# Kernel optimization log

Hardware: AMD Instinct MI355X
Metric: run time of the kernel (lower is better)

## Reference

```python
import jax, jax.numpy as jnp
import numpy as np

C, T, V, H, DQ = 64, 128, 25, 3, 32  # channels, frames, joints, heads, qkv_dim
EPS = 1e-5
LRELU_SLOPE = 0.1


def pos_embed(channels, num_frames, num_joints):
    # DSTA-Net style sinusoidal Pos_Embed: position index is the joint id, tiled over frames
    pos = np.tile(np.arange(num_joints, dtype=np.float32), num_frames)[:, None]  # (T*V, 1)
    div = np.exp(np.arange(0, channels, 2, dtype=np.float32) * -(np.log(10000.0) / channels))
    pe = np.zeros((num_frames * num_joints, channels), dtype=np.float32)
    pe[:, 0::2] = np.sin(pos * div)
    pe[:, 1::2] = np.cos(pos * div)
    pe = pe.reshape(num_frames, num_joints, channels).transpose(2, 0, 1)[None]  # (1, C, T, V)
    return jnp.asarray(pe)


def batchnorm2d(x, gamma, beta):
    # training-mode BN over (N, T, V) per channel, biased variance (torch default)
    m = x.mean(axis=(0, 2, 3), keepdims=True)
    v = x.var(axis=(0, 2, 3), keepdims=True)
    return (x - m) * jax.lax.rsqrt(v + EPS) * gamma[None, :, None, None] + beta[None, :, None, None]


def setup_inputs() -> dict:
    key = jax.random.key(0)
    ks = jax.random.split(key, 4)
    N = 64
    return {
        "x": jax.random.normal(ks[0], (N, C, T, V), jnp.float32),
        "Wqkv": jax.random.normal(ks[1], (2 * H * DQ, C), jnp.float32) * 0.05,   # 1x1 conv weight
        "bqkv": jnp.zeros((2 * H * DQ,), jnp.float32),
        "alphas": jnp.ones((1, H, 1, 1), jnp.float32),
        "att0s": jax.random.uniform(ks[2], (1, H, V, V), jnp.float32) / V,
        "Wout": jax.random.normal(ks[3], (C, H * C, 1, 5), jnp.float32) * 0.02,  # (1,5) temporal conv
        "bout": jnp.zeros((C,), jnp.float32),
        "gamma": jnp.ones((C,), jnp.float32),
        "beta": jnp.zeros((C,), jnp.float32),
    }


def reference(x, Wqkv, bqkv, alphas, att0s, Wout, bout, gamma, beta):
    N = x.shape[0]
    xs = x + pos_embed(C, T, V)                                   # pes(x) + x
    qk = jnp.einsum('nctv,oc->notv', xs, Wqkv) + bqkv[None, :, None, None]
    qk = qk.reshape(N, 2 * H, DQ, T, V)
    q, k = qk[:, :H], qk[:, H:]
    # tanh-gated joint-attention, no softmax
    att = jnp.tanh(jnp.einsum('nhctu,nhctv->nhuv', q, k) / (DQ * T)) * alphas + att0s
    y = jnp.einsum('nctu,nhuv->nhctv', x, att).reshape(N, H * C, T, V)
    y = jax.lax.conv_general_dilated(
        y, Wout, window_strides=(1, 1), padding=((0, 0), (2, 2)),
        dimension_numbers=('NCHW', 'OIHW', 'NCHW')) + bout[None, :, None, None]
    y = batchnorm2d(y, gamma, beta)
    return jax.nn.leaky_relu(y + x, LRELU_SLOPE)                  # ress is identity (in==out)
```

## Files before the change

kernel.cpp:

```cpp
#include <hip/hip_runtime.h>
#include <hip/hip_bf16.h>


#define WS_ATT    0
#define WS_STATS  120000
#define WS_WBF    120128
#define WS_WP     150848
#define WS_BP     156992
#define WS_PE     157184
#define WS_SPART  158784
#define WS_ATTBF  166976

typedef __attribute__((ext_vector_type(8))) short short8;
typedef __attribute__((ext_vector_type(4))) float floatx4;

__device__ __forceinline__ float us2f(unsigned short u) {
    union { unsigned int i; float f; } w; w.i = ((unsigned int)u) << 16; return w.f;
}
__device__ __forceinline__ unsigned short f2us(float f) {
    __hip_bfloat16_raw r = __float2bfloat16(f); return r.x;
}

__device__ __forceinline__ int swz(int col, int byteoff) {
    return col * 128 + ((((byteoff >> 4) ^ (col & 7)) << 4) | (byteoff & 15));
}

__device__ __forceinline__ void bar_lgkm() {
    asm volatile("s_waitcnt lgkmcnt(0)" ::: "memory");
    __builtin_amdgcn_s_barrier();
}

__global__ void k_wprep(const float* __restrict__ Wout, const float* __restrict__ Wqkv,
                        const float* __restrict__ bqkv, unsigned short* __restrict__ Abf,
                        unsigned short* __restrict__ Wp, float* __restrict__ bp,
                        float* __restrict__ pe)
{
    int i = blockIdx.x * 256 + threadIdx.x;
    if (i < 61440) {
        int tap = i / 12288, rem = i % 12288;
        int o = rem / 192, hc = rem % 192;
        Abf[i] = f2us(Wout[o * 960 + hc * 5 + tap]);
    } else if (i < 73728) {
        int j = i - 61440;
        int np = j >> 6, c = j & 63;
        int h = np >> 6, qk = (np >> 5) & 1, cp = np & 31;
        Wp[j] = f2us(Wqkv[(qk * 96 + h * 32 + cp) * 64 + c]);
    } else if (i < 73920) {
        int np = i - 73728;
        int h = np >> 6, qk = (np >> 5) & 1, cp = np & 31;
        bp[np] = bqkv[qk * 96 + h * 32 + cp];
    } else if (i < 75520) {
        int e = i - 73920;
        int c = e / 25, v = e % 25;
        int ii = c >> 1;
        float d = expf(-(float)(2 * ii) * (9.210340371976184f / 64.0f));
        float a = (float)v * d;
        pe[e] = (c & 1) ? cosf(a) : sinf(a);
    }
}

#define CPAD 112

__global__ __launch_bounds__(256, 2) void k_att(
    const float* __restrict__ x, const unsigned short* __restrict__ Wp,
    const float* __restrict__ bp, float* __restrict__ att_raw)
{
    __shared__ unsigned short xs_s[CPAD * 64];
    __shared__ unsigned short qk_s[3 * CPAD * 64];
    __shared__ float pe_s[1600];
    __shared__ float att_s[1875];

    const int tid  = threadIdx.x;
    const int lane = tid & 63, wv = tid >> 6;
    const int l16  = lane & 15, quad = lane >> 4;
    const int n    = blockIdx.y;
    const int tb0  = blockIdx.x * 16;

    for (int e = tid; e < 1600; e += 256) {
        int c = e / 25, v = e % 25;
        int i = c >> 1;
        float d = expf(-(float)(2 * i) * (9.210340371976184f / 64.0f));
        float a = (float)v * d;
        pe_s[e] = (c & 1) ? cosf(a) : sinf(a);
    }
    for (int e = tid; e < 1875; e += 256) att_s[e] = 0.0f;

    short8 afrag[3][2];
    float  biasr[3][4];
    #pragma unroll
    for (int mt = 0; mt < 3; ++mt) {
        int row = (3 * wv + mt) * 16 + l16;
        #pragma unroll
        for (int kk = 0; kk < 2; ++kk)
            afrag[mt][kk] = *(const short8*)(Wp + row * 64 + kk * 32 + quad * 8);
        #pragma unroll
        for (int reg = 0; reg < 4; ++reg)
            biasr[mt][reg] = bp[(3 * wv + mt) * 16 + quad * 4 + reg];
    }

    floatx4 qacc[3][2][2];
    #pragma unroll
    for (int h = 0; h < 3; ++h)
        #pragma unroll
        for (int a = 0; a < 2; ++a)
            #pragma unroll
            for (int b = 0; b < 2; ++b)
                qacc[h][a][b] = (floatx4){0.0f, 0.0f, 0.0f, 0.0f};

    const int col_a = lane;
    const int col_b = 64 + lane;
    const int va = (col_a < 25) ? col_a : (col_a < 50 ? col_a - 25 : col_a - 50);
    const int vb = (col_b < 75) ? col_b - 50 : col_b - 75;
    char* xsb = (char*)xs_s;
    char* qkb = (char*)qk_s;

    __syncthreads();

    for (int ch = 0; ch < 4; ++ch) {
        const int g0 = (tb0 + ch * 4) * 25;

        #pragma unroll
        for (int cp8 = 0; cp8 < 8; ++cp8) {
            const int cpair = wv * 8 + cp8;
            const int c0 = cpair * 2;
            const float* xp0 = x + (size_t)(n * 64 + c0) * 3200 + g0;
            const float* xp1 = xp0 + 3200;
            {
                unsigned int pk =
                    (unsigned int)f2us(xp0[col_a] + pe_s[c0 * 25 + va]) |
                    ((unsigned int)f2us(xp1[col_a] + pe_s[c0 * 25 + 25 + va]) << 16);
                *(unsigned int*)(xsb + swz(col_a, cpair * 4)) = pk;
            }
            if (lane < 36) {
                unsigned int pk =
                    (unsigned int)f2us(xp0[col_b] + pe_s[c0 * 25 + vb]) |
                    ((unsigned int)f2us(xp1[col_b] + pe_s[c0 * 25 + 25 + vb]) << 16);
                *(unsigned int*)(xsb + swz(col_b, cpair * 4)) = pk;
            }
        }
        __syncthreads();

        #pragma unroll
        for (int nt = 0; nt < 7; ++nt) {
            const int col = nt * 16 + l16;
            short8 b0 = *(const short8*)(xsb + swz(col, quad * 16));
            short8 b1 = *(const short8*)(xsb + swz(col, 64 + quad * 16));
            #pragma unroll
            for (int mt = 0; mt < 3; ++mt) {
                floatx4 acc = (floatx4){0.0f, 0.0f, 0.0f, 0.0f};
                acc = __builtin_amdgcn_mfma_f32_16x16x32_bf16(afrag[mt][0], b0, acc, 0, 0, 0);
                acc = __builtin_amdgcn_mfma_f32_16x16x32_bf16(afrag[mt][1], b1, acc, 0, 0, 0);
                const int np  = (3 * wv + mt) * 16 + quad * 4;
                const int h   = np >> 6;
                const int off = (np & 63) * 2;
                unsigned long long pk =
                      (unsigned long long)f2us(acc[0] + biasr[mt][0])
                    | ((unsigned long long)f2us(acc[1] + biasr[mt][1]) << 16)
                    | ((unsigned long long)f2us(acc[2] + biasr[mt][2]) << 32)
                    | ((unsigned long long)f2us(acc[3] + biasr[mt][3]) << 48);
                *(unsigned long long*)(qkb + h * (CPAD * 128) + swz(col, off)) = pk;
            }
        }
        __syncthreads();

        const int tcol = wv * 25;
        #pragma unroll
        for (int h = 0; h < 3; ++h) {
            char* qh = qkb + h * (CPAD * 128);
            short8 qa0 = *(const short8*)(qh + swz(tcol + l16,      quad * 16));
            short8 qa1 = *(const short8*)(qh + swz(tcol + 16 + l16, quad * 16));
            short8 kb0 = *(const short8*)(qh + swz(tcol + l16,      64 + quad * 16));
            short8 kb1 = *(const short8*)(qh + swz(tcol + 16 + l16, 64 + quad * 16));
            qacc[h][0][0] = __builtin_amdgcn_mfma_f32_16x16x32_bf16(qa0, kb0, qacc[h][0][0], 0, 0, 0);
            qacc[h][0][1] = __builtin_amdgcn_mfma_f32_16x16x32_bf16(qa0, kb1, qacc[h][0][1], 0, 0, 0);
            qacc[h][1][0] = __builtin_amdgcn_mfma_f32_16x16x32_bf16(qa1, kb0, qacc[h][1][0], 0, 0, 0);
            qacc[h][1][1] = __builtin_amdgcn_mfma_f32_16x16x32_bf16(qa1, kb1, qacc[h][1][1], 0, 0, 0);
        }
    }

    #pragma unroll
    for (int h = 0; h < 3; ++h) {
        #pragma unroll
        for (int ut = 0; ut < 2; ++ut) {
            #pragma unroll
            for (int vt = 0; vt < 2; ++vt) {
                const int v = vt * 16 + l16;
                if (v < 25) {
                    const int ub = ut * 16 + quad * 4;
                    #pragma unroll
                    for (int reg = 0; reg < 4; ++reg) {
                        const int u = ub + reg;
                        if (u < 25)
                            atomicAdd(&att_s[h * 625 + u * 25 + v], qacc[h][ut][vt][reg]);
                    }
                }
            }
        }
    }
    __syncthreads();
    for (int e = tid; e < 1875; e += 256)
        atomicAdd(&att_raw[(size_t)n * 1875 + e], att_s[e]);
}

__global__ void k_attfin(const float* __restrict__ att_raw,
                         unsigned short* __restrict__ attbf,
                         const float* __restrict__ alphas,
                         const float* __restrict__ att0s)
{
    int idx = blockIdx.x * 256 + threadIdx.x;
    if (idx >= 64 * 3 * 25 * 40) return;
    int u = idx % 40;
    int r = idx / 40;
    int v = r % 25;
    int nh = r / 25;
    int h = nh % 3;
    unsigned short val = 0;
    if (u < 25) {
        float a = att_raw[nh * 625 + u * 25 + v];
        val = f2us(tanhf(a * (1.0f / 4096.0f)) * alphas[h] + att0s[h * 625 + u * 25 + v]);
    }
    attbf[idx] = val;
}

__global__ __launch_bounds__(256, 3) void k_conv(
    const float* __restrict__ x, const unsigned short* __restrict__ Abf,
    const float* __restrict__ bout, const unsigned short* __restrict__ attbf,
    float* __restrict__ out, float* __restrict__ spart)
{
    __shared__ unsigned short yT[11136];
    __shared__ unsigned short x_sb[4096];
    __shared__ unsigned short attT[3000];
    __shared__ float stats_s[128];

    const int tid = threadIdx.x;
    const int n = blockIdx.y;
    const int t0 = blockIdx.x * 2;
    char* xsb = (char*)x_sb;

    if (tid < 128) stats_s[tid] = 0.0f;

    for (int e = tid; e < 896; e += 256) {
        int c = e / 14, r = e % 14;
        int t = r / 7, u = 25 + r % 7;
        *(unsigned short*)(xsb + swz(c, (t * 32 + u) * 2)) = 0;
    }
    for (int e = tid; e < 1600; e += 256) {
        int c = e / 25, j = e % 25;
        const float2 xv = *(const float2*)(x + (size_t)(n * 64 + c) * 3200 + t0 * 25 + 2 * j);
        int i0 = 2 * j, i1 = i0 + 1;
        int p0 = (i0 / 25) * 32 + (i0 % 25);
        int p1 = (i1 / 25) * 32 + (i1 % 25);
        *(unsigned short*)(xsb + swz(c, p0 * 2)) = f2us(xv.x);
        *(unsigned short*)(xsb + swz(c, p1 * 2)) = f2us(xv.y);
    }
    {
        const uint4* src = (const uint4*)(attbf + (size_t)n * 3000);
        uint4* dst = (uint4*)attT;
        for (int e = tid; e < 375; e += 256) dst[e] = src[e];
    }
    for (int e = tid; e < 1536; e += 256) {
        int t = e / 768, r = e % 768;
        int vi = r / 192, hc = r % 192;
        int vv = (vi < 2) ? vi : (25 + vi);
        int phys = (t * 29 + vv) * 192 + (((hc >> 3) ^ (vv & 7)) << 3) + (hc & 7);
        yT[phys] = 0;
    }
    __syncthreads();

    const int lane = tid & 63, wv = tid >> 6;
    const int quad = lane >> 4, l16 = lane & 15;

    {
        const int c0 = wv * 16;
        const int crow = c0 + l16;
        short8 af[2];
        #pragma unroll
        for (int t = 0; t < 2; ++t)
            af[t] = *(const short8*)(xsb + swz(crow, (t * 32 + quad * 8) * 2));
        short8 bfr[3][2];
        #pragma unroll
        for (int h = 0; h < 3; ++h)
            #pragma unroll
            for (int nt = 0; nt < 2; ++nt) {
                int v = nt * 16 + l16; if (v > 24) v = 24;
                bfr[h][nt] = *(const short8*)&attT[(h * 25 + v) * 40 + quad * 8];
            }
        #pragma unroll
        for (int t = 0; t < 2; ++t)
            #pragma unroll
            for (int h = 0; h < 3; ++h)
                #pragma unroll
                for (int nt = 0; nt < 2; ++nt) {
                    floatx4 d = (floatx4){0.0f, 0.0f, 0.0f, 0.0f};
                    d = __builtin_amdgcn_mfma_f32_16x16x32_bf16(af[t], bfr[h][nt], d, 0, 0, 0);
                    const int v = nt * 16 + l16;
                    if (v < 25) {
                        const int vv = v + 2;
                        const int hc = h * 64 + c0 + quad * 4;
                        const int phys = (t * 29 + vv) * 192 + (((hc >> 3) ^ (vv & 7)) << 3) + (hc & 7);
                        unsigned long long pk =
                              (unsigned long long)f2us(d[0])
                            | ((unsigned long long)f2us(d[1]) << 16)
                            | ((unsigned long long)f2us(d[2]) << 32)
                            | ((unsigned long long)f2us(d[3]) << 48);
                        *(unsigned long long*)&yT[phys] = pk;
                    }
                }
    }

    const int o0 = wv * 16;
    short8 areg[5][6];
    const unsigned short* apb = Abf + (o0 + l16) * 192 + quad * 8;
    #pragma unroll
    for (int tap = 0; tap < 5; ++tap)
        #pragma unroll
        for (int kk = 0; kk < 6; ++kk)
            areg[tap][kk] = *(const short8*)(apb + tap * 12288 + kk * 32);
    float bo[4];
    #pragma unroll
    for (int reg = 0; reg < 4; ++reg) bo[reg] = bout[o0 + quad * 4 + reg];

    bar_lgkm();

    float s1[4] = {0, 0, 0, 0}, s2[4] = {0, 0, 0, 0};
    #pragma unroll
    for (int nt = 0; nt < 4; ++nt) {
        int col = nt * 16 + l16;
        const bool ok = col < 50;
        if (col > 49) col = 49;
        const int tc = col / 25, vc = col % 25;
        floatx4 acc = (floatx4){0.0f, 0.0f, 0.0f, 0.0f};
        #pragma unroll
        for (int tap = 0; tap < 5; ++tap) {
            const int vv = vc + tap;
            const int ro = (tc * 29 + vv) * 192, vx = vv & 7;
            #pragma unroll
            for (int kk = 0; kk < 6; ++kk) {
                short8 b = *(const short8*)&yT[ro + (((kk * 4 + quad) ^ vx) << 3)];
                acc = __builtin_amdgcn_mfma_f32_16x16x32_bf16(areg[tap][kk], b, acc, 0, 0, 0);
            }
        }
        float vr[4];
        #pragma unroll
        for (int reg = 0; reg < 4; ++reg)
            vr[reg] = ok ? acc[reg] + bo[reg] : 0.0f;
        if (ok) {
            float* op = out + (size_t)(n * 64 + o0 + quad * 4) * 3200 + (t0 + tc) * 25 + vc;
            #pragma unroll
            for (int reg = 0; reg < 4; ++reg)
                op[(size_t)reg * 3200] = vr[reg];
        }
        #pragma unroll
        for (int reg = 0; reg < 4; ++reg) {
            s1[reg] += vr[reg];
            s2[reg] = fmaf(vr[reg], vr[reg], s2[reg]);
        }
    }

    #pragma unroll
    for (int reg = 0; reg < 4; ++reg) {
        float a = s1[reg], b = s2[reg];
        #pragma unroll
        for (int m = 1; m < 16; m <<= 1) {
            a += __shfl_xor(a, m);
            b += __shfl_xor(b, m);
        }
        if (l16 == 0) {
            atomicAdd(&stats_s[o0 + quad * 4 + reg], a);
            atomicAdd(&stats_s[64 + o0 + quad * 4 + reg], b);
        }
    }
    __syncthreads();
    if (tid < 128)
        atomicAdd(&spart[(size_t)blockIdx.x * 128 + tid], stats_s[tid]);
}

__global__ void k_statsred(const float* __restrict__ spart, float* __restrict__ stats)
{
    int o = threadIdx.x;
    float s = 0.0f;
    #pragma unroll 8
    for (int t = 0; t < 64; ++t) s += spart[t * 128 + o];
    stats[o] = s;
}

__global__ void k_final(const float* __restrict__ stats, const float4* __restrict__ x4,
                        const float* __restrict__ gamma, const float* __restrict__ beta,
                        float4* __restrict__ out4)
{
    int idx = blockIdx.x * 256 + threadIdx.x;
    if (idx >= 3276800) return;
    int o = (idx / 800) & 63;
    const float inv = 1.0f / 204800.0f;
    float m   = stats[o] * inv;
    float ex2 = stats[64 + o] * inv;
    float var = ex2 - m * m;
    float r = rsqrtf(var + 1e-5f);
    float g = gamma[o], bb = beta[o];
    float4 v = out4[idx];
    float4 xx = x4[idx];
    float4 res;
    float t;
    t = (v.x - m) * r * g + bb + xx.x; res.x = fmaxf(t, 0.1f * t);
    t = (v.y - m) * r * g + bb + xx.y; res.y = fmaxf(t, 0.1f * t);
    t = (v.z - m) * r * g + bb + xx.z; res.z = fmaxf(t, 0.1f * t);
    t = (v.w - m) * r * g + bb + xx.w; res.w = fmaxf(t, 0.1f * t);
    out4[idx] = res;
}

extern "C" void kernel_launch(void* const* d_in, const int* in_sizes, int n_in,
                              void* d_out, int out_size, void* d_ws, size_t ws_size,
                              hipStream_t stream)
{
    const float* x      = (const float*)d_in[0];
    const float* Wqkv   = (const float*)d_in[1];
    const float* bqkv   = (const float*)d_in[2];
    const float* alphas = (const float*)d_in[3];
    const float* att0s  = (const float*)d_in[4];
    const float* Wout   = (const float*)d_in[5];
    const float* bout   = (const float*)d_in[6];
    const float* gamma  = (const float*)d_in[7];
    const float* beta   = (const float*)d_in[8];
    float* ws  = (float*)d_ws;
    float* out = (float*)d_out;
    unsigned short* Abf   = (unsigned short*)(ws + WS_WBF);
    unsigned short* Wp    = (unsigned short*)(ws + WS_WP);
    float*          bp    = ws + WS_BP;
    float*          pe    = ws + WS_PE;
    float*          spart = ws + WS_SPART;
    unsigned short* attbf = (unsigned short*)(ws + WS_ATTBF);

    hipMemsetAsync(d_ws, 0, (size_t)120000 * sizeof(float), stream);
    hipMemsetAsync(spart, 0, (size_t)8192 * sizeof(float), stream);

    k_wprep   <<<296, 256, 0, stream>>>(Wout, Wqkv, bqkv, Abf, Wp, bp, pe);
    k_att     <<<dim3(8, 64),  256, 0, stream>>>(x, Wp, bp, ws + WS_ATT);
    k_attfin  <<<750, 256, 0, stream>>>(ws + WS_ATT, attbf, alphas, att0s);
    k_conv    <<<dim3(64, 64), 256, 0, stream>>>(x, Abf, bout, attbf, out, spart);
    k_statsred<<<1, 128, 0, stream>>>(spart, ws + WS_STATS);
    k_final   <<<12800, 256, 0, stream>>>(ws + WS_STATS, (const float4*)x,
                                          gamma, beta, (float4*)out);
}
```

Before: 294.5 us.

## Shrink k_att shared memory, preload positional embedding, double grid for occupancy

```diff
diff --git a/kernel.cpp b/kernel.cpp
--- a/kernel.cpp
+++ b/kernel.cpp
@@ -59,53 +59,21 @@
     }
 }
 
-#define CPAD 112
-
-__global__ __launch_bounds__(256, 2) void k_att(
+#define CPAD 104
+
+__global__ __launch_bounds__(256, 3) void k_att(
     const float* __restrict__ x, const unsigned short* __restrict__ Wp,
-    const float* __restrict__ bp, float* __restrict__ att_raw)
+    const float* __restrict__ bp, const float* __restrict__ peg,
+    float* __restrict__ att_raw)
 {
     __shared__ unsigned short xs_s[CPAD * 64];
     __shared__ unsigned short qk_s[3 * CPAD * 64];
-    __shared__ float pe_s[1600];
-    __shared__ float att_s[1875];
 
     const int tid  = threadIdx.x;
     const int lane = tid & 63, wv = tid >> 6;
     const int l16  = lane & 15, quad = lane >> 4;
     const int n    = blockIdx.y;
-    const int tb0  = blockIdx.x * 16;
-
-    for (int e = tid; e < 1600; e += 256) {
-        int c = e / 25, v = e % 25;
-        int i = c >> 1;
-        float d = expf(-(float)(2 * i) * (9.210340371976184f / 64.0f));
-        float a = (float)v * d;
-        pe_s[e] = (c & 1) ? cosf(a) : sinf(a);
-    }
-    for (int e = tid; e < 1875; e += 256) att_s[e] = 0.0f;
-
-    short8 afrag[3][2];
-    float  biasr[3][4];
-    #pragma unroll
-    for (int mt = 0; mt < 3; ++mt) {
-        int row = (3 * wv + mt) * 16 + l16;
-        #pragma unroll
-        for (int kk = 0; kk < 2; ++kk)
-            afrag[mt][kk] = *(const short8*)(Wp + row * 64 + kk * 32 + quad * 8);
-        #pragma unroll
-        for (int reg = 0; reg < 4; ++reg)
-            biasr[mt][reg] = bp[(3 * wv + mt) * 16 + quad * 4 + reg];
-    }
-
-    floatx4 qacc[3][2][2];
-    #pragma unroll
-    for (int h = 0; h < 3; ++h)
-        #pragma unroll
-        for (int a = 0; a < 2; ++a)
-            #pragma unroll
-            for (int b = 0; b < 2; ++b)
-                qacc[h][a][b] = (floatx4){0.0f, 0.0f, 0.0f, 0.0f};
+    const int tb0  = blockIdx.x * 8;
 
     const int col_a = lane;
     const int col_b = 64 + lane;
@@ -114,9 +82,44 @@
     char* xsb = (char*)xs_s;
     char* qkb = (char*)qk_s;
 
-    __syncthreads();
-
-    for (int ch = 0; ch < 4; ++ch) {
+    float pea[16], peb[16];
+    #pragma unroll
+    for (int k = 0; k < 16; ++k) {
+        const int c = (wv * 8 + (k >> 1)) * 2 + (k & 1);
+        pea[k] = peg[c * 25 + va];
+    }
+    if (lane < 36) {
+        #pragma unroll
+        for (int k = 0; k < 16; ++k) {
+            const int c = (wv * 8 + (k >> 1)) * 2 + (k & 1);
+            peb[k] = peg[c * 25 + vb];
+        }
+    }
+
+    short8 afrag[3][2];
+    float  biasr[3][4];
+    #pragma unroll
+    for (int mt = 0; mt < 3; ++mt) {
+        int row = (3 * wv + mt) * 16 + l16;
+        #pragma unroll
+        for (int kk = 0; kk < 2; ++kk)
+            afrag[mt][kk] = *(const short8*)(Wp + row * 64 + kk * 32 + quad * 8);
+        #pragma unroll
+        for (int reg = 0; reg < 4; ++reg)
+            biasr[mt][reg] = bp[(3 * wv + mt) * 16 + quad * 4 + reg];
+    }
+
+    floatx4 qacc[3][2][2];
+    #pragma unroll
+    for (int h = 0; h < 3; ++h)
+        #pragma unroll
+        for (int a = 0; a < 2; ++a)
+            #pragma unroll
+            for (int b = 0; b < 2; ++b)
+                qacc[h][a][b] = (floatx4){0.0f, 0.0f, 0.0f, 0.0f};
+
+    #pragma unroll
+    for (int ch = 0; ch < 2; ++ch) {
         const int g0 = (tb0 + ch * 4) * 25;
 
         #pragma unroll
@@ -127,57 +130,66 @@
             const float* xp1 = xp0 + 3200;
             {
                 unsigned int pk =
-                    (unsigned int)f2us(xp0[col_a] + pe_s[c0 * 25 + va]) |
-                    ((unsigned int)f2us(xp1[col_a] + pe_s[c0 * 25 + 25 + va]) << 16);
+                    (unsigned int)f2us(xp0[col_a] + pea[2 * cp8]) |
+                    ((unsigned int)f2us(xp1[col_a] + pea[2 * cp8 + 1]) << 16);
                 *(unsigned int*)(xsb + swz(col_a, cpair * 4)) = pk;
             }
             if (lane < 36) {
                 unsigned int pk =
-                    (unsigned int)f2us(xp0[col_b] + pe_s[c0 * 25 + vb]) |
-                    ((unsigned int)f2us(xp1[col_b] + pe_s[c0 * 25 + 25 + vb]) << 16);
+                    (unsigned int)f2us(xp0[col_b] + peb[2 * cp8]) |
+                    ((unsigned int)f2us(xp1[col_b] + peb[2 * cp8 + 1]) << 16);
                 *(unsigned int*)(xsb + swz(col_b, cpair * 4)) = pk;
             }
         }
-        __syncthreads();
+        bar_lgkm();
 
         #pragma unroll
         for (int nt = 0; nt < 7; ++nt) {
             const int col = nt * 16 + l16;
-            short8 b0 = *(const short8*)(xsb + swz(col, quad * 16));
-            short8 b1 = *(const short8*)(xsb + swz(col, 64 + quad * 16));
+            const int colr = (col > 99) ? 99 : col;
+            short8 b0 = *(const short8*)(xsb + swz(colr, quad * 16));
+            short8 b1 = *(const short8*)(xsb + swz(colr, 64 + quad * 16));
             #pragma unroll
             for (int mt = 0; mt < 3; ++mt) {
                 floatx4 acc = (floatx4){0.0f, 0.0f, 0.0f, 0.0f};
                 acc = __builtin_amdgcn_mfma_f32_16x16x32_bf16(afrag[mt][0], b0, acc, 0, 0, 0);
                 acc = __builtin_amdgcn_mfma_f32_16x16x32_bf16(afrag[mt][1], b1, acc, 0, 0, 0);
-                const int np  = (3 * wv + mt) * 16 + quad * 4;
-                const int h   = np >> 6;
-                const int off = (np & 63) * 2;
-                unsigned long long pk =
-                      (unsigned long long)f2us(acc[0] + biasr[mt][0])
-                    | ((unsigned long long)f2us(acc[1] + biasr[mt][1]) << 16)
-                    | ((unsigned long long)f2us(acc[2] + biasr[mt][2]) << 32)
-                    | ((unsigned long long)f2us(acc[3] + biasr[mt][3]) << 48);
-                *(unsigned long long*)(qkb + h * (CPAD * 128) + swz(col, off)) = pk;
-            }
-        }
-        __syncthreads();
+                if (col < 100) {
+                    const int np  = (3 * wv + mt) * 16 + quad * 4;
+                    const int h   = np >> 6;
+                    const int off = (np & 63) * 2;
+                    unsigned long long pk =
+                          (unsigned long long)f2us(acc[0] + biasr[mt][0])
+                        | ((unsigned long long)f2us(acc[1] + biasr[mt][1]) << 16)
+                        | ((unsigned long long)f2us(acc[2] + biasr[mt][2]) << 32)
+                        | ((unsigned long long)f2us(acc[3] + biasr[mt][3]) << 48);
+                    *(unsigned long long*)(qkb + h * (CPAD * 128) + swz(col, off)) = pk;
+                }
+            }
+        }
+        bar_lgkm();
 
         const int tcol = wv * 25;
+        int chi = tcol + 16 + l16; if (chi > 99) chi = 99;
         #pragma unroll
         for (int h = 0; h < 3; ++h) {
             char* qh = qkb + h * (CPAD * 128);
-            short8 qa0 = *(const short8*)(qh + swz(tcol + l16,      quad * 16));
-            short8 qa1 = *(const short8*)(qh + swz(tcol + 16 + l16, quad * 16));
-            short8 kb0 = *(const short8*)(qh + swz(tcol + l16,      64 + quad * 16));
-            short8 kb1 = *(const short8*)(qh + swz(tcol + 16 + l16, 64 + quad * 16));
+            short8 qa0 = *(const short8*)(qh + swz(tcol + l16, quad * 16));
+            short8 qa1 = *(const short8*)(qh + swz(chi,        quad * 16));
+            short8 kb0 = *(const short8*)(qh + swz(tcol + l16, 64 + quad * 16));
+            short8 kb1 = *(const short8*)(qh + swz(chi,        64 + quad * 16));
             qacc[h][0][0] = __builtin_amdgcn_mfma_f32_16x16x32_bf16(qa0, kb0, qacc[h][0][0], 0, 0, 0);
             qacc[h][0][1] = __builtin_amdgcn_mfma_f32_16x16x32_bf16(qa0, kb1, qacc[h][0][1], 0, 0, 0);
             qacc[h][1][0] = __builtin_amdgcn_mfma_f32_16x16x32_bf16(qa1, kb0, qacc[h][1][0], 0, 0, 0);
             qacc[h][1][1] = __builtin_amdgcn_mfma_f32_16x16x32_bf16(qa1, kb1, qacc[h][1][1], 0, 0, 0);
         }
-    }
-
+        bar_lgkm();
+    }
+
+    __syncthreads();
+    float* att_s = (float*)qk_s;
+    for (int e = tid; e < 1875; e += 256) att_s[e] = 0.0f;
+    __syncthreads();
     #pragma unroll
     for (int h = 0; h < 3; ++h) {
         #pragma unroll
@@ -434,7 +446,7 @@
     hipMemsetAsync(spart, 0, (size_t)8192 * sizeof(float), stream);
 
     k_wprep   <<<296, 256, 0, stream>>>(Wout, Wqkv, bqkv, Abf, Wp, bp, pe);
-    k_att     <<<dim3(8, 64),  256, 0, stream>>>(x, Wp, bp, ws + WS_ATT);
+    k_att     <<<dim3(16, 64), 256, 0, stream>>>(x, Wp, bp, pe, ws + WS_ATT);
     k_attfin  <<<750, 256, 0, stream>>>(ws + WS_ATT, attbf, alphas, att0s);
     k_conv    <<<dim3(64, 64), 256, 0, stream>>>(x, Abf, bout, attbf, out, spart);
     k_statsred<<<1, 128, 0, stream>>>(spart, ws + WS_STATS);
```

Result: slower. 340.3 us (+15.6%).
